# Optimization experiments

Measured on AMD Instinct MI355X. Metric: run time of the kernel, lower is better.

## Reference

```python
import jax, jax.numpy as jnp
import numpy as np

NCHARS = 50000
NWORDS = 500000
NIC = 64      # ninput_char
NIW = 64      # ninput_word
NH = 128      # nhidden
NA = 5        # naction (nmapping_fn)
B = 65536     # batch size


def setup_inputs() -> dict:
    key = jax.random.key(0)
    ks = jax.random.split(key, 12)
    s = 0.05
    return {
        "x": jax.random.randint(ks[0], (B, 2), 0, NCHARS),
        "y": jax.random.randint(ks[1], (B,), 0, NWORDS),
        "cemb_table": jax.random.normal(ks[2], (NCHARS, NIC), jnp.float32) * s,
        "wemb_table": jax.random.normal(ks[3], (NWORDS, NIW), jnp.float32) * s,
        # Policy MLP: Linear(2*NIC -> NH), ReLU, Linear(NH -> NA), Softmax
        "Wp1": jax.random.normal(ks[4], (2 * NIC, NH), jnp.float32) * s,
        "bp1": jnp.zeros((NH,), jnp.float32),
        "Wp2": jax.random.normal(ks[5], (NH, NA), jnp.float32) * s,
        "bp2": jnp.zeros((NA,), jnp.float32),
        # NA expert MLPs, stacked: Linear(2*NIC -> NH), ReLU, Linear(NH -> NIW)
        "We1": jax.random.normal(ks[6], (NA, 2 * NIC, NH), jnp.float32) * s,
        "be1": jnp.zeros((NA, NH), jnp.float32),
        "We2": jax.random.normal(ks[7], (NA, NH, NIW), jnp.float32) * s,
        "be2": jnp.zeros((NA, NIW), jnp.float32),
    }


def reference(x, y, cemb_table, wemb_table, Wp1, bp1, Wp2, bp2, We1, be1, We2, be2):
    bsize = x.shape[0]
    # char_embs(x).view(bsize, -1): [B, 2*NIC]
    cembs = cemb_table[x].reshape(bsize, -1)

    # Policy (dropout off in eval): probs = softmax(relu(cembs@Wp1+bp1)@Wp2+bp2)
    # Categorical sampling over probs == categorical over the pre-softmax logits.
    logits = jnp.maximum(cembs @ Wp1 + bp1, 0.0) @ Wp2 + bp2
    action = jax.random.categorical(jax.random.key(42), logits)   # [B]
    action_mask = jax.nn.one_hot(action, NA, dtype=cembs.dtype)   # [B, NA]

    # Dense evaluation of all NA experts (matches the Python loop + stack)
    h = jnp.maximum(jnp.einsum('bd,adh->bah', cembs, We1) + be1, 0.0)  # [B, NA, NH]
    mapped = jnp.einsum('bah,aho->bao', h, We2) + be2                  # [B, NA, NIW]

    # sum(unsqueeze(mask,-1) * mapped, dim=1)
    out = jnp.einsum('ba,bao->bo', action_mask, mapped)               # [B, NIW]

    wemb = wemb_table[y]                                              # [B, NIW]
    return (out, wemb)
```

## Files before the change

kernel.cpp:

```cpp
#include <hip/hip_runtime.h>
#include <stdint.h>

#define B_N   65536
#define NIC   64
#define NIW   64
#define NH    128
#define NA    5
#define D2    128

#define PARTITIONABLE 1

#define NBLK      512
#define P2_NCHUNK 51
#define P2_R      1286

#define WS_ACTION_BYTES  262144

typedef __attribute__((ext_vector_type(8))) short short8;
typedef __attribute__((ext_vector_type(4))) float f32x4;

__device__ __forceinline__ ushort f2bf(float f) {
  uint32_t u = __float_as_uint(f);
  uint32_t r = (u + 0x7FFFu + ((u >> 16) & 1u)) >> 16;
  return (ushort)r;
}

__device__ __forceinline__ void split2(float f, ushort& h, ushort& l) {
  h = f2bf(f);
  l = f2bf(f - __uint_as_float(((uint32_t)h) << 16));
}

__device__ __forceinline__ void threefry2x32_k042(uint32_t x0, uint32_t x1,
                                                  uint32_t& o0, uint32_t& o1) {
  const uint32_t ks0 = 0u;
  const uint32_t ks1 = 42u;
  const uint32_t ks2 = 0x1BD11BDAu ^ 0u ^ 42u;
  x0 += ks0; x1 += ks1;
#define TF_RND(r) { x0 += x1; x1 = (x1 << (r)) | (x1 >> (32 - (r))); x1 ^= x0; }
  TF_RND(13) TF_RND(15) TF_RND(26) TF_RND(6)
  x0 += ks1; x1 += ks2 + 1u;
  TF_RND(17) TF_RND(29) TF_RND(16) TF_RND(24)
  x0 += ks2; x1 += ks0 + 2u;
  TF_RND(13) TF_RND(15) TF_RND(26) TF_RND(6)
  x0 += ks0; x1 += ks1 + 3u;
  TF_RND(17) TF_RND(29) TF_RND(16) TF_RND(24)
  x0 += ks1; x1 += ks2 + 4u;
  TF_RND(13) TF_RND(15) TF_RND(26) TF_RND(6)
  x0 += ks2; x1 += ks0 + 5u;
#undef TF_RND
  o0 = x0; o1 = x1;
}

__device__ __forceinline__ float gumbel_at(uint32_t idx) {
  uint32_t bits;
#if PARTITIONABLE
  uint32_t a, b;
  threefry2x32_k042(0u, idx, a, b);
  bits = a ^ b;
#else
  const uint32_t HALF = (uint32_t)(B_N * NA) / 2u;
  uint32_t a, b;
  if (idx < HALF) { threefry2x32_k042(idx, idx + HALF, a, b); bits = a; }
  else            { threefry2x32_k042(idx - HALF, idx, a, b); bits = b; }
#endif
  const float f = __uint_as_float((bits >> 9) | 0x3f800000u) - 1.0f;
  const double u = (f == 0.0f) ? (double)0x1p-126 : (double)f;
  const float nl = (float)(-log(u));
  const float g  = (float)(-log((double)nl));
  return g;
}

__global__ __launch_bounds__(512, 4) void policy_kernel(
    const int* __restrict__ x, const int* __restrict__ y,
    const float* __restrict__ cemb, const float* __restrict__ wemb,
    const float* __restrict__ Wp1, const float* __restrict__ bp1,
    const float* __restrict__ Wp2, const float* __restrict__ bp2,
    const float* __restrict__ We1, const float* __restrict__ We2,
    float* __restrict__ out_wemb, int* __restrict__ action,
    ushort* __restrict__ wPrep) {
  __shared__ __align__(16) ushort sW1h[16384];
  __shared__ __align__(16) ushort sW1l[16384];
  __shared__ __align__(16) float sW2t[NA][NH];
  __shared__ __align__(16) float sb1[NH];
  __shared__ __align__(16) float sbp2[8];

  const int tid = threadIdx.x;

  if (blockIdx.x >= NBLK) {
    const int a = blockIdx.x - NBLK;
    ushort* wp = wPrep + (size_t)a * 24576;
    {
      const float* W1g = We1 + (size_t)a * D2 * NH;
      const int n = tid & 127, q = tid >> 7;
      const int fb = (n >> 4) * 4 + q;
      const int cc = n & 15;
#pragma unroll
      for (int grp = 0; grp < 4; grp++) {
        short8 pk;
#pragma unroll
        for (int j = 0; j < 8; j++)
          pk[j] = (short)f2bf(W1g[(32 * q + 8 * grp + j) * NH + n]);
        *(short8*)&wp[fb * 512 + (cc + 16 * grp) * 8] = pk;
      }
    }
    {
      const float* W2g = We2 + (size_t)a * NH * NIW;
      const int o = tid & 63, hq = tid >> 6;
      const int fb = (o >> 4) * 4 + (hq >> 1);
      const int cc = o & 15;
#pragma unroll
      for (int g2 = 0; g2 < 2; g2++) {
        const int grp = (hq & 1) * 2 + g2;
        short8 pk;
#pragma unroll
        for (int j = 0; j < 8; j++)
          pk[j] = (short)f2bf(W2g[(16 * hq + 8 * g2 + j) * NIW + o]);
        *(short8*)&wp[16384 + fb * 512 + (cc + 16 * grp) * 8] = pk;
      }
    }
    return;
  }

  const int base = blockIdx.x * 128;

  {
    const int n = tid & 127, q = tid >> 7;
    const int fb = (n >> 4) * 4 + q;
    const int cc = n & 15;
#pragma unroll
    for (int grp = 0; grp < 4; grp++) {
      short8 ph, pl;
#pragma unroll
      for (int j = 0; j < 8; j++) {
        const int k = 32 * q + 8 * grp + j;
        ushort hh, ll;
        split2(Wp1[k * NH + n], hh, ll);
        ph[j] = (short)hh;
        pl[j] = (short)ll;
      }
      *(short8*)&sW1h[fb * 512 + (cc + 16 * grp) * 8] = ph;
      *(short8*)&sW1l[fb * 512 + (cc + 16 * grp) * 8] = pl;
    }
    if (tid < NH) sb1[tid] = bp1[tid];
    if (tid < NA * 32) {
      const int a = tid >> 5, k0 = (tid & 31) * 4;
#pragma unroll
      for (int j = 0; j < 4; j++) sW2t[a][k0 + j] = Wp2[(k0 + j) * NA + a];
    }
    if (tid < NA) sbp2[tid] = bp2[tid];
  }

  const int wave = tid >> 6, lane = tid & 63;
  const int c16 = lane & 15, h2 = lane >> 4;

  const int grow = base + wave * 16 + c16;
  const int2 xi2p = ((const int2*)x)[grow];
  const int xi0 = xi2p.x, xi1 = xi2p.y;
  short8 Ah[4], Al[4];
#pragma unroll
  for (int kt = 0; kt < 4; kt++) {
    const int xi = (kt < 2) ? xi0 : xi1;
    const float* src = cemb + (size_t)xi * NIC + (kt & 1) * 32 + h2 * 8;
    const float4 aa = *(const float4*)src;
    const float4 bb = *(const float4*)(src + 4);
    ushort hh, ll;
    short8 ph, pl;
    split2(aa.x, hh, ll); ph[0] = (short)hh; pl[0] = (short)ll;
    split2(aa.y, hh, ll); ph[1] = (short)hh; pl[1] = (short)ll;
    split2(aa.z, hh, ll); ph[2] = (short)hh; pl[2] = (short)ll;
    split2(aa.w, hh, ll); ph[3] = (short)hh; pl[3] = (short)ll;
    split2(bb.x, hh, ll); ph[4] = (short)hh; pl[4] = (short)ll;
    split2(bb.y, hh, ll); ph[5] = (short)hh; pl[5] = (short)ll;
    split2(bb.z, hh, ll); ph[6] = (short)hh; pl[6] = (short)ll;
    split2(bb.w, hh, ll); ph[7] = (short)hh; pl[7] = (short)ll;
    Ah[kt] = ph;
    Al[kt] = pl;
  }
  __syncthreads();

  float part[4][5];
#pragma unroll
  for (int r = 0; r < 4; r++)
#pragma unroll
    for (int a = 0; a < NA; a++) part[r][a] = 0.0f;

#pragma unroll
  for (int half = 0; half < 2; half++) {
    f32x4 acc[4];
#pragma unroll
    for (int c2 = 0; c2 < 4; c2++) {
      const float bv = sb1[(half * 4 + c2) * 16 + c16];
      acc[c2] = (f32x4){bv, bv, bv, bv};
    }
#pragma unroll
    for (int kt = 0; kt < 4; kt++) {
#pragma unroll
      for (int c2 = 0; c2 < 4; c2++) {
        const int fb = (half * 4 + c2) * 4 + kt;
        const short8 Bh = *(const short8*)&sW1h[fb * 512 + lane * 8];
        const short8 Bl = *(const short8*)&sW1l[fb * 512 + lane * 8];
        acc[c2] = __builtin_amdgcn_mfma_f32_16x16x32_bf16(Ah[kt], Bh, acc[c2], 0, 0, 0);
        acc[c2] = __builtin_amdgcn_mfma_f32_16x16x32_bf16(Al[kt], Bh, acc[c2], 0, 0, 0);
        acc[c2] = __builtin_amdgcn_mfma_f32_16x16x32_bf16(Ah[kt], Bl, acc[c2], 0, 0, 0);
      }
    }
#pragma unroll
    for (int c2 = 0; c2 < 4; c2++) {
      const int ct = half * 4 + c2;
      float w[NA];
#pragma unroll
      for (int a = 0; a < NA; a++) w[a] = sW2t[a][ct * 16 + c16];
#pragma unroll
      for (int r = 0; r < 4; r++) {
        const float hv = fmaxf(acc[c2][r], 0.0f);
#pragma unroll
        for (int a = 0; a < NA; a++) part[r][a] = fmaf(hv, w[a], part[r][a]);
      }
    }
  }

#pragma unroll
  for (int st = 1; st <= 8; st <<= 1) {
#pragma unroll
    for (int r = 0; r < 4; r++)
#pragma unroll
      for (int a = 0; a < NA; a++)
        part[r][a] += __shfl_xor(part[r][a], st);
  }

  float score0, score1;
  {
    const int r0_ = c16 / 5, a0_ = c16 - 5 * (c16 / 5);
    float lg = 0.0f;
#pragma unroll
    for (int r = 0; r < 4; r++)
#pragma unroll
      for (int a = 0; a < NA; a++)
        if (r0_ == r && a0_ == a) lg = part[r][a];
    const float logit = lg + sbp2[a0_];
    const int growr = base + wave * 16 + h2 * 4 + r0_;
    score0 = gumbel_at((uint32_t)(growr * NA + a0_)) + logit;
  }
  {
    const int a1_ = (c16 & 3) + 1;
    float lg = 0.0f;
#pragma unroll
    for (int a = 1; a < NA; a++)
      if (a1_ == a) lg = part[3][a];
    const float logit = lg + sbp2[a1_];
    const int growr = base + wave * 16 + h2 * 4 + 3;
    score1 = gumbel_at((uint32_t)(growr * NA + a1_)) + logit;
  }

  int best = 0;
  float bs = 0.0f;
#pragma unroll
  for (int a = 0; a < NA; a++) {
    const int idx = c16 * 5 + a;
    const int src = h2 * 16 + ((idx < 16) ? idx : (idx - 16));
    const float v0 = __shfl(score0, src);
    const float v1 = __shfl(score1, src);
    const float s = (idx < 16) ? v0 : v1;
    if (a == 0) bs = s;
    else if (s > bs) { bs = s; best = a; }
  }
  if (c16 < 4) action[base + wave * 16 + h2 * 4 + c16] = best;

#pragma unroll 1
  for (int i = tid; i < 128 * 16; i += 512) {
    const int row = i >> 4, seg = i & 15;
    ((float4*)out_wemb)[(size_t)(base + row) * 16 + seg] =
        ((const float4*)wemb)[(size_t)y[base + row] * 16 + seg];
  }
}

__global__ __launch_bounds__(512, 1) void expert_staged(
    const int* __restrict__ x, const float* __restrict__ cemb,
    const float* __restrict__ be1, const float* __restrict__ be2,
    const int* __restrict__ action, const ushort* __restrict__ wPrep,
    float* __restrict__ out) {
  __shared__ __align__(16) ushort sW1[16384];
  __shared__ __align__(16) ushort sW2[8192];
  __shared__ __align__(16) ushort sHt[8][2048];
  __shared__ __align__(16) float sbe1[NH];
  __shared__ __align__(16) float sbe2[NIW];
  __shared__ int sList[P2_R];
  __shared__ int sCount;

  const int tid = threadIdx.x;
  const int a = blockIdx.x % NA;
  const int chunk = blockIdx.x / NA;
  const int rowBeg = chunk * P2_R;
  const int rowEnd = (rowBeg + P2_R < B_N) ? rowBeg + P2_R : B_N;

  const int wave = tid >> 6, lane = tid & 63;

  if (tid == 0) sCount = 0;
  __syncthreads();

  {
    const short8* s1 = (const short8*)(wPrep + (size_t)a * 24576);
    const short8* s2 = s1 + 2048;
    short8* d1 = (short8*)sW1;
    short8* d2 = (short8*)sW2;
#pragma unroll
    for (int i = 0; i < 4; i++) d1[tid + i * 512] = s1[tid + i * 512];
#pragma unroll
    for (int i = 0; i < 2; i++) d2[tid + i * 512] = s2[tid + i * 512];
    if (tid < NH) sbe1[tid] = be1[a * NH + tid];
    if (tid < NIW) sbe2[tid] = be2[a * NIW + tid];
  }

  for (int r0 = rowBeg; r0 < rowEnd; r0 += 512) {
    const int r = r0 + tid;
    const bool m = (r < rowEnd) && (action[r] == a);
    const unsigned long long mask = __ballot(m);
    const int wcnt = __popcll(mask);
    int wbase = 0;
    if (lane == 0 && wcnt) wbase = atomicAdd(&sCount, wcnt);
    wbase = __shfl(wbase, 0);
    if (m)
      sList[wbase + __popcll(mask & ((1ull << lane) - 1ull))] = r;
  }
  __syncthreads();

  const int cnt = sCount;
  if (cnt == 0) return;

  const int c16 = lane & 15, h2 = lane >> 4;
  const int rowb = h2 * 4;
  ushort* myHt = sHt[wave];

  int t16 = wave * 16;
  if (t16 >= cnt) return;

  float4 raw[8];
  {
    const int slot = t16 + c16;
    const int g = sList[(slot < cnt) ? slot : 0];
    const int2 xi2 = ((const int2*)x)[g];
#pragma unroll
    for (int kt = 0; kt < 4; kt++) {
      const float* src = cemb + (size_t)((kt < 2) ? xi2.x : xi2.y) * NIC +
                         (kt & 1) * 32 + h2 * 8;
      raw[2 * kt]     = *(const float4*)src;
      raw[2 * kt + 1] = *(const float4*)(src + 4);
    }
  }

#pragma unroll 1
  while (t16 < cnt) {
    const int tn = t16 + 128;

    short8 Ae[4];
#pragma unroll
    for (int kt = 0; kt < 4; kt++) {
      const float4 aa = raw[2 * kt], bb = raw[2 * kt + 1];
      short8 pk;
      pk[0] = (short)f2bf(aa.x); pk[1] = (short)f2bf(aa.y);
      pk[2] = (short)f2bf(aa.z); pk[3] = (short)f2bf(aa.w);
      pk[4] = (short)f2bf(bb.x); pk[5] = (short)f2bf(bb.y);
      pk[6] = (short)f2bf(bb.z); pk[7] = (short)f2bf(bb.w);
      Ae[kt] = pk;
    }

    if (tn < cnt) {
      const int slot = tn + c16;
      const int g = sList[(slot < cnt) ? slot : 0];
      const int2 xi2 = ((const int2*)x)[g];
#pragma unroll
      for (int kt = 0; kt < 4; kt++) {
        const float* src = cemb + (size_t)((kt < 2) ? xi2.x : xi2.y) * NIC +
                           (kt & 1) * 32 + h2 * 8;
        raw[2 * kt]     = *(const float4*)src;
        raw[2 * kt + 1] = *(const float4*)(src + 4);
      }
    }

#pragma unroll
    for (int ct = 0; ct < 8; ct++) {
      const int n = ct * 16 + c16;
      const float bv = sbe1[n];
      f32x4 acc = {bv, bv, bv, bv};
#pragma unroll
      for (int kt = 0; kt < 4; kt++) {
        const short8 Bf = *(const short8*)&sW1[(ct * 4 + kt) * 512 + lane * 8];
        acc = __builtin_amdgcn_mfma_f32_16x16x32_bf16(Ae[kt], Bf, acc, 0, 0, 0);
      }
      const int kt2 = n >> 5, grp2 = (n & 31) >> 3, j2 = n & 7;
#pragma unroll
      for (int r = 0; r < 4; r++)
        myHt[kt2 * 512 + ((rowb + r) + 16 * grp2) * 8 + j2] =
            f2bf(fmaxf(acc[r], 0.0f));
    }

    short8 A2[4];
#pragma unroll
    for (int kt = 0; kt < 4; kt++)
      A2[kt] = *(const short8*)&myHt[kt * 512 + lane * 8];
    int gr4[4];
#pragma unroll
    for (int r = 0; r < 4; r++) {
      const int li2 = t16 + rowb + r;
      gr4[r] = (li2 < cnt) ? sList[li2] : -1;
    }
#pragma unroll
    for (int ot = 0; ot < 4; ot++) {
      const int o = ot * 16 + c16;
      const float bv = sbe2[o];
      f32x4 o4 = {bv, bv, bv, bv};
#pragma unroll
      for (int kt = 0; kt < 4; kt++) {
        const short8 Bf = *(const short8*)&sW2[(ot * 4 + kt) * 512 + lane * 8];
        o4 = __builtin_amdgcn_mfma_f32_16x16x32_bf16(A2[kt], Bf, o4, 0, 0, 0);
      }
#pragma unroll
      for (int r = 0; r < 4; r++)
        if (gr4[r] >= 0) out[(size_t)gr4[r] * NIW + o] = o4[r];
    }

    t16 = tn;
  }
}

extern "C" void kernel_launch(void* const* d_in, const int* in_sizes, int n_in,
                              void* d_out, int out_size, void* d_ws, size_t ws_size,
                              hipStream_t stream) {
  const int*   x    = (const int*)d_in[0];
  const int*   y    = (const int*)d_in[1];
  const float* cemb = (const float*)d_in[2];
  const float* wemb = (const float*)d_in[3];
  const float* Wp1  = (const float*)d_in[4];
  const float* bp1  = (const float*)d_in[5];
  const float* Wp2  = (const float*)d_in[6];
  const float* bp2  = (const float*)d_in[7];
  const float* We1  = (const float*)d_in[8];
  const float* be1  = (const float*)d_in[9];
  const float* We2  = (const float*)d_in[10];
  const float* be2  = (const float*)d_in[11];

  float* out      = (float*)d_out;
  float* out_wemb = out + (size_t)B_N * NIW;
  int*    action  = (int*)d_ws;
  ushort* wPrep   = (ushort*)((char*)d_ws + WS_ACTION_BYTES);

  policy_kernel<<<NBLK + NA, 512, 0, stream>>>(
      x, y, cemb, wemb, Wp1, bp1, Wp2, bp2, We1, We2, out_wemb, action, wPrep);
  expert_staged<<<NA * P2_NCHUNK, 512, 0, stream>>>(
      x, cemb, be1, be2, action, wPrep, out);
}
```

Before: 42.21 us.

## Build per-expert compacted row lists in policy kernel via global atomics

The policy kernel now buckets each block's sampled actions into per-expert lists in shared memory. It reserves a slot range with one global atomic per expert and writes the global row indices into a workspace list. The expert kernel no longer scans the action array and ballot-compacts its row range. Instead, each chunk block copies an even share of its expert's precompacted list, which should also balance work across chunks. The cost is a memset launch to zero the counters, extra atomics and syncs in the policy kernel, and a nondeterministic row order within each expert list.

```diff
diff --git a/kernel.cpp b/kernel.cpp
--- a/kernel.cpp
+++ b/kernel.cpp
@@ -14,7 +14,8 @@
 #define P2_NCHUNK 51
 #define P2_R      1286
 
-#define WS_ACTION_BYTES  262144
+#define WS_GLIST_OFF   4096
+#define WS_PREP_OFF    (WS_GLIST_OFF + NA * B_N * 4)
 
 typedef __attribute__((ext_vector_type(8))) short short8;
 typedef __attribute__((ext_vector_type(4))) float f32x4;
@@ -76,13 +77,16 @@
     const float* __restrict__ Wp1, const float* __restrict__ bp1,
     const float* __restrict__ Wp2, const float* __restrict__ bp2,
     const float* __restrict__ We1, const float* __restrict__ We2,
-    float* __restrict__ out_wemb, int* __restrict__ action,
-    ushort* __restrict__ wPrep) {
+    float* __restrict__ out_wemb, int* __restrict__ gcnt,
+    int* __restrict__ glist, ushort* __restrict__ wPrep) {
   __shared__ __align__(16) ushort sW1h[16384];
   __shared__ __align__(16) ushort sW1l[16384];
   __shared__ __align__(16) float sW2t[NA][NH];
   __shared__ __align__(16) float sb1[NH];
   __shared__ __align__(16) float sbp2[8];
+  __shared__ ushort sBList[NA][128];
+  __shared__ int sBCnt[NA];
+  __shared__ int sBase[8];
 
   const int tid = threadIdx.x;
 
@@ -148,6 +152,7 @@
       for (int j = 0; j < 4; j++) sW2t[a][k0 + j] = Wp2[(k0 + j) * NA + a];
     }
     if (tid < NA) sbp2[tid] = bp2[tid];
+    if (tid < NA) sBCnt[tid] = 0;
   }
 
   const int wave = tid >> 6, lane = tid & 63;
@@ -264,7 +269,20 @@
     if (a == 0) bs = s;
     else if (s > bs) { bs = s; best = a; }
   }
-  if (c16 < 4) action[base + wave * 16 + h2 * 4 + c16] = best;
+  if (c16 < 4) {
+    const int rl = wave * 16 + h2 * 4 + c16;
+    const int p = atomicAdd(&sBCnt[best], 1);
+    sBList[best][p] = (ushort)rl;
+  }
+  __syncthreads();
+  if (tid < NA) sBase[tid] = atomicAdd(&gcnt[tid], sBCnt[tid]);
+  __syncthreads();
+#pragma unroll
+  for (int a = 0; a < NA; a++) {
+    const int c = sBCnt[a], gb = sBase[a];
+    for (int i = tid; i < c; i += 512)
+      glist[a * B_N + gb + i] = base + (int)sBList[a][i];
+  }
 
 #pragma unroll 1
   for (int i = tid; i < 128 * 16; i += 512) {
@@ -277,26 +295,25 @@
 __global__ __launch_bounds__(512, 1) void expert_staged(
     const int* __restrict__ x, const float* __restrict__ cemb,
     const float* __restrict__ be1, const float* __restrict__ be2,
-    const int* __restrict__ action, const ushort* __restrict__ wPrep,
-    float* __restrict__ out) {
+    const int* __restrict__ gcnt, const int* __restrict__ glist,
+    const ushort* __restrict__ wPrep, float* __restrict__ out) {
   __shared__ __align__(16) ushort sW1[16384];
   __shared__ __align__(16) ushort sW2[8192];
   __shared__ __align__(16) ushort sHt[8][2048];
   __shared__ __align__(16) float sbe1[NH];
   __shared__ __align__(16) float sbe2[NIW];
   __shared__ int sList[P2_R];
-  __shared__ int sCount;
 
   const int tid = threadIdx.x;
   const int a = blockIdx.x % NA;
   const int chunk = blockIdx.x / NA;
-  const int rowBeg = chunk * P2_R;
-  const int rowEnd = (rowBeg + P2_R < B_N) ? rowBeg + P2_R : B_N;
-
-  const int wave = tid >> 6, lane = tid & 63;
-
-  if (tid == 0) sCount = 0;
-  __syncthreads();
+
+  const int cnt_a = gcnt[a];
+  const int len = (cnt_a + P2_NCHUNK - 1) / P2_NCHUNK;
+  const int beg = chunk * len;
+  int scnt = cnt_a - beg;
+  if (scnt > len) scnt = len;
+  if (scnt < 0) scnt = 0;
 
   {
     const short8* s1 = (const short8*)(wPrep + (size_t)a * 24576);
@@ -310,34 +327,26 @@
     if (tid < NH) sbe1[tid] = be1[a * NH + tid];
     if (tid < NIW) sbe2[tid] = be2[a * NIW + tid];
   }
-
-  for (int r0 = rowBeg; r0 < rowEnd; r0 += 512) {
-    const int r = r0 + tid;
-    const bool m = (r < rowEnd) && (action[r] == a);
-    const unsigned long long mask = __ballot(m);
-    const int wcnt = __popcll(mask);
-    int wbase = 0;
-    if (lane == 0 && wcnt) wbase = atomicAdd(&sCount, wcnt);
-    wbase = __shfl(wbase, 0);
-    if (m)
-      sList[wbase + __popcll(mask & ((1ull << lane) - 1ull))] = r;
+  {
+    const int* gsrc = glist + a * B_N + beg;
+    for (int i = tid; i < scnt; i += 512) sList[i] = gsrc[i];
   }
   __syncthreads();
 
-  const int cnt = sCount;
-  if (cnt == 0) return;
-
+  if (scnt == 0) return;
+
+  const int wave = tid >> 6, lane = tid & 63;
   const int c16 = lane & 15, h2 = lane >> 4;
   const int rowb = h2 * 4;
   ushort* myHt = sHt[wave];
 
   int t16 = wave * 16;
-  if (t16 >= cnt) return;
+  if (t16 >= scnt) return;
 
   float4 raw[8];
   {
     const int slot = t16 + c16;
-    const int g = sList[(slot < cnt) ? slot : 0];
+    const int g = sList[(slot < scnt) ? slot : 0];
     const int2 xi2 = ((const int2*)x)[g];
 #pragma unroll
     for (int kt = 0; kt < 4; kt++) {
@@ -349,7 +358,7 @@
   }
 
 #pragma unroll 1
-  while (t16 < cnt) {
+  while (t16 < scnt) {
     const int tn = t16 + 128;
 
     short8 Ae[4];
@@ -364,9 +373,9 @@
       Ae[kt] = pk;
     }
 
-    if (tn < cnt) {
+    if (tn < scnt) {
       const int slot = tn + c16;
-      const int g = sList[(slot < cnt) ? slot : 0];
+      const int g = sList[(slot < scnt) ? slot : 0];
       const int2 xi2 = ((const int2*)x)[g];
 #pragma unroll
       for (int kt = 0; kt < 4; kt++) {
@@ -402,7 +411,7 @@
 #pragma unroll
     for (int r = 0; r < 4; r++) {
       const int li2 = t16 + rowb + r;
-      gr4[r] = (li2 < cnt) ? sList[li2] : -1;
+      gr4[r] = (li2 < scnt) ? sList[li2] : -1;
     }
 #pragma unroll
     for (int ot = 0; ot < 4; ot++) {
@@ -441,11 +450,14 @@
 
   float* out      = (float*)d_out;
   float* out_wemb = out + (size_t)B_N * NIW;
-  int*    action  = (int*)d_ws;
-  ushort* wPrep   = (ushort*)((char*)d_ws + WS_ACTION_BYTES);
-
+  int*    gcnt  = (int*)d_ws;
+  int*    glist = (int*)((char*)d_ws + WS_GLIST_OFF);
+  ushort* wPrep = (ushort*)((char*)d_ws + WS_PREP_OFF);
+
+  hipMemsetAsync(d_ws, 0, WS_GLIST_OFF, stream);
   policy_kernel<<<NBLK + NA, 512, 0, stream>>>(
-      x, y, cemb, wemb, Wp1, bp1, Wp2, bp2, We1, We2, out_wemb, action, wPrep);
+      x, y, cemb, wemb, Wp1, bp1, Wp2, bp2, We1, We2,
+      out_wemb, gcnt, glist, wPrep);
   expert_staged<<<NA * P2_NCHUNK, 512, 0, stream>>>(
-      x, cemb, be1, be2, action, wPrep, out);
-}
+      x, cemb, be1, be2, gcnt, glist, wPrep, out);
+}
```

Result: slower. 48.85 us (+15.7%).
